# Kernel optimization log

Measured on AMD Instinct MI355X. Metric: run time of the kernel, lower is better.

Reference implementation:

```python
import jax, jax.numpy as jnp
import numpy as np

B, L, E, H = 8, 2048, 1024, 16
D = E // H
EPS = 1e-6


def setup_inputs() -> dict:
    key = jax.random.key(0)
    ks = jax.random.split(key, 9)
    s = 1.0 / np.sqrt(E)
    def lin_w(k):
        return jax.random.uniform(k, (E, E), jnp.float32, -s, s)
    def lin_b(k):
        return jax.random.uniform(k, (E,), jnp.float32, -s, s)
    return {
        "query": jax.random.normal(ks[0], (B, L, E), jnp.float32),
        "Wq": lin_w(ks[1]), "bq": lin_b(ks[2]),
        "Wk": lin_w(ks[3]), "bk": lin_b(ks[4]),
        "Wv": lin_w(ks[5]), "bv": lin_b(ks[6]),
        "Wo": lin_w(ks[7]), "bo": lin_b(ks[8]),
    }


def reference(query, Wq, bq, Wk, bk, Wv, bv, Wo, bo):
    bsz, tgt_len, embed_dim = query.shape
    n_head = H
    head_dim = embed_dim // n_head
    m = tgt_len  # src_len == tgt_len (self-attention)

    # projections (torch Linear with W stored as (in, out) here)
    q = query @ Wq + bq
    k = query @ Wk + bk
    v = query @ Wv + bv

    # (B, L, E) -> (B, H, L, D), softmax feature map over head dim
    def to_heads(x):
        return x.reshape(bsz, tgt_len, n_head, head_dim).transpose(0, 2, 1, 3)

    q = jax.nn.softmax(to_heads(q), axis=-1)
    k = jax.nn.softmax(to_heads(k), axis=-1)
    v = to_heads(v)
    comp_q = 1.0 - q
    comp_k = 1.0 - k

    # cosFormer positional reweighting: idx = (pi/2) * (1..m) / m
    idx = (np.pi / 2) * jnp.arange(1, m + 1, dtype=jnp.float32) / m  # (L,)
    sin = jnp.sin(idx)[None, None, :, None]  # (1,1,L,1)
    cos = jnp.cos(idx)[None, None, :, None]

    def feat(x):  # (B,H,L,D) -> (B,H,L,2D)
        return jnp.concatenate([x * sin, x * cos], axis=-1)

    qf, comp_qf = feat(q), feat(comp_q)
    kf, comp_kf = feat(k), feat(comp_k)

    def branch(qf_, kf_):
        kv = jnp.einsum('bhld,bhlm->bhdm', kf_, v)            # (B,H,2D,D)
        z = 1.0 / jnp.maximum(
            jnp.einsum('bhld,bhd->bhl', qf_, kf_.sum(axis=2)), EPS)
        return jnp.einsum('bhld,bhdm,bhl->bhlm', qf_, kv, z)  # (B,H,L,D)

    attn = branch(qf, kf) + branch(comp_qf, comp_kf)

    # torch: (B*H,L,D).transpose(0,1).view(L,B,E)
    out = attn.transpose(2, 0, 1, 3).reshape(tgt_len, bsz, embed_dim)
    out = out @ Wo + bo
    # torch final: .view(bsz, tgt_len, n_feat) -- raw reshape, no transpose
    return out.reshape(bsz, tgt_len, embed_dim)
```

## Files before the change

kernel.cpp:

```cpp
#include <hip/hip_runtime.h>
#include <hip/hip_bf16.h>
#include <cstdint>

#define B_   8
#define L_   2048
#define E_   1024
#define H_   16
#define D_   64
#define M_   (B_ * L_)
#define EPS_ 1e-6f
#define PI2_ 1.57079632679f

typedef __bf16 bf16;
typedef __bf16 bf16x8 __attribute__((ext_vector_type(8)));
typedef __bf16 bf16x4 __attribute__((ext_vector_type(4)));
typedef float  floatx4 __attribute__((ext_vector_type(4)));

__device__ inline void async_cp16(const void* g, void* l) {
  __builtin_amdgcn_global_load_lds(
      (__attribute__((address_space(1))) void*)const_cast<void*>(g),
      (__attribute__((address_space(3))) void*)l,
      16, 0, 0);
}

__global__ __launch_bounds__(256) void k_convert_x(const float* __restrict__ x,
                                                   bf16* __restrict__ o) {
  size_t i = ((size_t)blockIdx.x * 256 + threadIdx.x) * 8;
  floatx4 a = *(const floatx4*)(x + i);
  floatx4 b = *(const floatx4*)(x + i + 4);
  bf16x8 r;
  r[0] = (bf16)a[0]; r[1] = (bf16)a[1]; r[2] = (bf16)a[2]; r[3] = (bf16)a[3];
  r[4] = (bf16)b[0]; r[5] = (bf16)b[1]; r[6] = (bf16)b[2]; r[7] = (bf16)b[3];
  *(bf16x8*)(o + i) = r;
}

struct TArgs { const float* src[4]; bf16* dst[4]; };

__global__ __launch_bounds__(256) void k_transpose_w(TArgs t) {
  __shared__ float tile[32][33];
  const float* src = t.src[blockIdx.z];
  bf16* dst = t.dst[blockIdx.z];
  int bx = blockIdx.x, by = blockIdx.y;
  int x = threadIdx.x, y = threadIdx.y;
#pragma unroll
  for (int i = 0; i < 4; i++) {
    int r = by * 32 + y + i * 8;
    tile[y + i * 8][x] = src[(size_t)r * E_ + bx * 32 + x];
  }
  __syncthreads();
#pragma unroll
  for (int i = 0; i < 4; i++) {
    int r = bx * 32 + y + i * 8;
    dst[(size_t)r * E_ + by * 32 + x] = (bf16)tile[x][y + i * 8];
  }
}

#define BAR()   asm volatile("s_barrier" ::: "memory")
#define LGKM0() asm volatile("s_waitcnt lgkmcnt(0)" ::: "memory")
#define VMW4()  asm volatile("s_waitcnt vmcnt(4)" ::: "memory")
#define VMW0()  asm volatile("s_waitcnt vmcnt(0)" ::: "memory")
#define MFMA_   __builtin_amdgcn_mfma_f32_16x16x32_bf16

#define GEMM_TILE(t_, c_) {                                                    \
    const int t = (t_); const int c = (c_);                                    \
    bf16x8 a0[4][2], a1[4][2], b0[2][2], b1[2][2];                             \
                                                                  \
    _Pragma("unroll") for (int i = 0; i < 4; i++) {                            \
      a0[i][0] = RDA(c, 0, i); a0[i][1] = RDA(c, 1, i); }                      \
    _Pragma("unroll") for (int j = 0; j < 2; j++) {                            \
      b0[j][0] = RDB(c, 0, j); b0[j][1] = RDB(c, 1, j); }                      \
    if (t + 1 < 16) STAGE(c ^ 1, 0, t + 1, 0);                                 \
    BAR(); LGKM0();                                                            \
    __builtin_amdgcn_s_setprio(1);                                             \
    _Pragma("unroll") for (int i = 0; i < 4; i++)                              \
      _Pragma("unroll") for (int j = 0; j < 2; j++) {                          \
        acc[i][j] = MFMA_(a0[i][0], b0[j][0], acc[i][j], 0, 0, 0);             \
        acc[i][j] = MFMA_(a0[i][1], b0[j][1], acc[i][j], 0, 0, 0); }           \
    __builtin_amdgcn_s_setprio(0);                                             \
    BAR();                                                                     \
                                                                  \
    _Pragma("unroll") for (int j = 0; j < 2; j++) {                            \
      b1[j][0] = RDB(c, 0, j + 2); b1[j][1] = RDB(c, 1, j + 2); }              \
    if (t + 1 < 16) STAGE(c ^ 1, 0, t + 1, 1);                                 \
    BAR(); LGKM0();                                                            \
    __builtin_amdgcn_s_setprio(1);                                             \
    _Pragma("unroll") for (int i = 0; i < 4; i++)                              \
      _Pragma("unroll") for (int j = 0; j < 2; j++) {                          \
        acc[i][j + 2] = MFMA_(a0[i][0], b1[j][0], acc[i][j + 2], 0, 0, 0);     \
        acc[i][j + 2] = MFMA_(a0[i][1], b1[j][1], acc[i][j + 2], 0, 0, 0); }   \
    __builtin_amdgcn_s_setprio(0);                                             \
    BAR();                                                                     \
                                                                  \
    _Pragma("unroll") for (int i = 0; i < 4; i++) {                            \
      a1[i][0] = RDA(c, 0, i + 4); a1[i][1] = RDA(c, 1, i + 4); }              \
    if (t + 2 < 16) STAGE(c, 1, t + 2, 0);                                     \
    BAR(); LGKM0();                                                            \
    __builtin_amdgcn_s_setprio(1);                                             \
    _Pragma("unroll") for (int i = 0; i < 4; i++)                              \
      _Pragma("unroll") for (int j = 0; j < 2; j++) {                          \
        acc[i + 4][j + 2] = MFMA_(a1[i][0], b1[j][0], acc[i + 4][j + 2], 0, 0, 0); \
        acc[i + 4][j + 2] = MFMA_(a1[i][1], b1[j][1], acc[i + 4][j + 2], 0, 0, 0); } \
    __builtin_amdgcn_s_setprio(0);                                             \
    BAR();                                                                     \
                                                                  \
    if (t < 14) { STAGE(c, 1, t + 2, 1); VMW4(); } else { VMW0(); }            \
    BAR();                                                                     \
    __builtin_amdgcn_s_setprio(1);                                             \
    _Pragma("unroll") for (int i = 0; i < 4; i++)                              \
      _Pragma("unroll") for (int j = 0; j < 2; j++) {                          \
        acc[i + 4][j] = MFMA_(a1[i][0], b0[j][0], acc[i + 4][j], 0, 0, 0);     \
        acc[i + 4][j] = MFMA_(a1[i][1], b0[j][1], acc[i + 4][j], 0, 0, 0); }   \
    __builtin_amdgcn_s_setprio(0);                                             \
    BAR();                                                                     \
  }

__device__ __forceinline__ void gemm256_core(const bf16* __restrict__ Agl,
                                             const bf16* __restrict__ Bgl,
                                             int bm, int bn, bf16* ldsb,
                                             floatx4 (&acc)[8][4]) {
  const int tid  = threadIdx.x;
  const int wid  = tid >> 6;
  const int lane = tid & 63;
  const int quad = lane >> 4;
  const int l15  = lane & 15;
  const int wm   = wid >> 2;
  const int wn   = wid & 3;
  const int rb   = wn * 32;
  const int gcol = wm * 32 + (((lane & 3) * 8) ^ ((lane & 32) ? 16 : 0));
  const bf16* pA = Agl + (size_t)(bm * 256 + rb + (lane >> 2)) * E_ + gcol;
  const bf16* pB = Bgl + (size_t)(bn * 256 + rb + (lane >> 2)) * E_ + gcol;
  const int aCol = (quad * 8) ^ ((l15 & 8) ? 16 : 0);

  auto LDSP = [&](int c, int mat, int qq, int row, int col) -> bf16* {
    return ldsb + ((((c * 2 + mat) * 2 + qq) * 256 + row) * 32 + col);
  };
  auto STAGE = [&](int c, int mat, int tt, int h) {
    const bf16* g = (mat ? pB : pA) + (size_t)(h * 128) * E_ + tt * 64;
    bf16* lp = LDSP(c, mat, wm, h * 128 + rb, 0);
    async_cp16(g, lp);
    async_cp16(g + (size_t)16 * E_, lp + 16 * 32);
  };
  auto RDA = [&](int c, int qq, int i) -> bf16x8 {
    return *(const bf16x8*)LDSP(c, 0, qq, wm * 128 + i * 16 + l15, aCol);
  };
  auto RDB = [&](int c, int qq, int j) -> bf16x8 {
    return *(const bf16x8*)LDSP(c, 1, qq, wn * 64 + j * 16 + l15, aCol);
  };

  STAGE(0, 1, 0, 0); STAGE(0, 1, 0, 1);
  STAGE(0, 0, 0, 0); STAGE(0, 0, 0, 1);
  STAGE(1, 1, 1, 0); STAGE(1, 1, 1, 1);
  VMW4();
  BAR();

#pragma unroll 1
  for (int tb = 0; tb < 16; tb += 2) {
    GEMM_TILE(tb, 0)
    GEMM_TILE(tb + 1, 1)
  }
}

__global__ __launch_bounds__(512, 2) void k_gemm_qkv256(
    const bf16* __restrict__ A, const bf16* __restrict__ Wt,
    const float* __restrict__ bq, const float* __restrict__ bk,
    const float* __restrict__ bv,
    float* __restrict__ QT, float* __restrict__ KT, bf16* __restrict__ VT) {
  __shared__ __attribute__((aligned(16))) bf16 ldsb[2 * 2 * 2 * 256 * 32];
  const int id  = blockIdx.x;
  const int xcd = id & 7, rr = id >> 3;
  const int bm  = xcd * 8 + rr / 12;
  const int cz  = rr % 12;
  const int bn  = cz & 3, z = cz >> 2;
  const bf16* Bgl = Wt + (size_t)z * E_ * E_;

  floatx4 acc[8][4] = {};
  gemm256_core(A, Bgl, bm, bn, ldsb, acc);

  const int tid  = threadIdx.x;
  const int wid  = tid >> 6;
  const int lane = tid & 63;
  const int quad = lane >> 4;
  const int l15  = lane & 15;
  const int wm   = wid >> 2, wn = wid & 3;
  const float* bias = (z == 0) ? bq : (z == 1) ? bk : bv;
#pragma unroll
  for (int i = 0; i < 8; i++)
#pragma unroll
    for (int j = 0; j < 4; j++) {
      const int col  = bn * 256 + wn * 64 + j * 16 + l15;
      const int row0 = bm * 256 + wm * 128 + i * 16 + quad * 4;
      const int h = col >> 6, d = col & 63;
      const int b = row0 >> 11, l = row0 & 2047;
      const float bb = bias[col];
      floatx4 v = acc[i][j];
      v[0] += bb; v[1] += bb; v[2] += bb; v[3] += bb;
      if (z == 0) {
        *(floatx4*)&QT[(((size_t)(b * 16 + h) * 64 + d) * 2048) + l] = v;
      } else if (z == 1) {
        *(floatx4*)&KT[(((size_t)(b * 16 + h) * 64 + d) * 2048) + l] = v;
      } else {
        bf16x4 rv;
        rv[0] = (bf16)v[0]; rv[1] = (bf16)v[1];
        rv[2] = (bf16)v[2]; rv[3] = (bf16)v[3];
        *(bf16x4*)&VT[(((size_t)(b * 16 + h) * 64 + d) * 2048) + l] = rv;
      }
    }
}

__global__ __launch_bounds__(512, 2) void k_gemm_final256(
    const bf16* __restrict__ A, const bf16* __restrict__ Bt,
    const float* __restrict__ bias, float* __restrict__ C) {
  __shared__ __attribute__((aligned(16))) bf16 ldsb[2 * 2 * 2 * 256 * 32];
  const int id  = blockIdx.x;
  const int xcd = id & 7, rr = id >> 3;
  const int bm  = xcd * 8 + (rr >> 2);
  const int bn  = rr & 3;

  floatx4 acc[8][4] = {};
  gemm256_core(A, Bt, bm, bn, ldsb, acc);

  const int tid  = threadIdx.x;
  const int wid  = tid >> 6;
  const int lane = tid & 63;
  const int quad = lane >> 4;
  const int l15  = lane & 15;
  const int wm   = wid >> 2, wn = wid & 3;
#pragma unroll
  for (int i = 0; i < 8; i++)
#pragma unroll
    for (int j = 0; j < 4; j++) {
      const int col = bn * 256 + wn * 64 + j * 16 + l15;
      const float bb = bias[col];
#pragma unroll
      for (int r = 0; r < 4; r++) {
        const int row = bm * 256 + wm * 128 + i * 16 + quad * 4 + r;
        C[(size_t)row * E_ + col] = acc[i][j][r] + bb;
      }
    }
}

#define AST 40
__global__ __launch_bounds__(256) void k_kv(const float* __restrict__ KT,
                                            const bf16* __restrict__ VT,
                                            float* __restrict__ kvp) {
  __shared__ __attribute__((aligned(16))) float kt[64 * 32];
  __shared__ __attribute__((aligned(16))) bf16  vt[64 * 32];
  __shared__ __attribute__((aligned(16))) bf16  Abuf[128 * AST];
  const int kseg = blockIdx.x;
  const int bh   = blockIdx.y;
  const int t = threadIdx.x;
  const int wid = t >> 6, lane = t & 63;
  const int quad = lane >> 4, l15 = lane & 15;
  const int wm = wid >> 1, wn = wid & 1;
  const int c = t >> 3, ii = t & 7;

  const float* ktg = KT + (size_t)bh * 64 * 2048;
  const bf16*  vtg = VT + (size_t)bh * 64 * 2048;

  floatx4 acc[4][2] = {};
  float rs = 0.f;

  for (int it = 0; it < 16; it++) {
    const int l0 = kseg * 512 + it * 32;
    {
      const int r = lane >> 3, ch = lane & 7;
      const float* g0 = ktg + (size_t)(wid * 16 + r) * 2048 + l0 + ch * 4;
      const float* g1 = ktg + (size_t)(wid * 16 + 8 + r) * 2048 + l0 + ch * 4;
      async_cp16(g0, &kt[(wid * 16) * 32]);
      async_cp16(g1, &kt[(wid * 16 + 8) * 32]);
    }
    {
      const int r = lane >> 2, ch = lane & 3;
      const bf16* g0 = vtg + (size_t)(wid * 16 + r) * 2048 + l0 + ch * 8;
      async_cp16(g0, &vt[(wid * 16) * 32]);
    }
    __syncthreads();

    float xv[8];
#pragma unroll
    for (int j = 0; j < 8; j++) xv[j] = kt[(ii + 8 * j) * 32 + c];
    float mx = xv[0];
#pragma unroll
    for (int j = 1; j < 8; j++) mx = fmaxf(mx, xv[j]);
    mx = fmaxf(mx, __shfl_xor(mx, 1));
    mx = fmaxf(mx, __shfl_xor(mx, 2));
    mx = fmaxf(mx, __shfl_xor(mx, 4));
    float s = 0.f;
#pragma unroll
    for (int j = 0; j < 8; j++) { xv[j] = __expf(xv[j] - mx); s += xv[j]; }
    s += __shfl_xor(s, 1); s += __shfl_xor(s, 2); s += __shfl_xor(s, 4);
    const float inv = 1.f / s;
    const int l = l0 + c;
    const float ang = PI2_ * (float)(l + 1) / (float)L_;
    const float sn = __sinf(ang), cs = __cosf(ang);
#pragma unroll
    for (int j = 0; j < 8; j++) {
      const float p = xv[j] * inv;
      const int f = ii + 8 * j;
      Abuf[f * AST + c]        = (bf16)(p * sn);
      Abuf[(64 + f) * AST + c] = (bf16)(p * cs);
    }
    __syncthreads();

    if (t < 128) {
      float r8 = 0.f;
#pragma unroll
      for (int g = 0; g < 4; g++) {
        bf16x8 v = *(const bf16x8*)&Abuf[t * AST + g * 8];
#pragma unroll
        for (int e = 0; e < 8; e++) r8 += (float)v[e];
      }
      rs += r8;
    }

    bf16x8 af[4], bfm[2];
#pragma unroll
    for (int i = 0; i < 4; i++)
      af[i] = *(const bf16x8*)&Abuf[(wm * 64 + i * 16 + l15) * AST + quad * 8];
#pragma unroll
    for (int j = 0; j < 2; j++)
      bfm[j] = *(const bf16x8*)&vt[(wn * 32 + j * 16 + l15) * 32 + quad * 8];
#pragma unroll
    for (int i = 0; i < 4; i++)
#pragma unroll
      for (int j = 0; j < 2; j++)
        acc[i][j] = __builtin_amdgcn_mfma_f32_16x16x32_bf16(af[i], bfm[j], acc[i][j], 0, 0, 0);
    __syncthreads();
  }

  float* C = kvp + (size_t)(kseg * 128 + bh) * 128 * 68;
#pragma unroll
  for (int i = 0; i < 4; i++)
#pragma unroll
    for (int j = 0; j < 2; j++) {
      const int col = wn * 32 + j * 16 + l15;
#pragma unroll
      for (int r = 0; r < 4; r++) {
        const int row = wm * 64 + i * 16 + quad * 4 + r;
        C[(size_t)row * 68 + col] = acc[i][j][r];
      }
    }
  if (t < 128) C[(size_t)t * 68 + 64] = rs;
}

__global__ __launch_bounds__(64) void k_consts(const float* __restrict__ kvp,
                                               bf16* __restrict__ KVT,
                                               float* __restrict__ ksbuf) {
  const int bh = blockIdx.x;
  const int dp = threadIdx.x;
  const size_t gs = (size_t)128 * 128 * 68;
  const float* P = kvp + (size_t)bh * 128 * 68;
  bf16* kr = KVT + (size_t)(bh * 64 + dp) * 160;
  float sk0 = 0.f, sk1 = 0.f;
#pragma unroll 8
  for (int f = 0; f < 128; f++) {
    float v = P[(size_t)f * 68 + dp] + P[gs + (size_t)f * 68 + dp]
            + P[2 * gs + (size_t)f * 68 + dp] + P[3 * gs + (size_t)f * 68 + dp];
    kr[f] = (bf16)v;
    if (f < 64) sk0 += v; else sk1 += v;
  }
  float ks0 = P[(size_t)dp * 68 + 64] + P[gs + (size_t)dp * 68 + 64]
            + P[2 * gs + (size_t)dp * 68 + 64] + P[3 * gs + (size_t)dp * 68 + 64];
  float ks1 = P[(size_t)(64 + dp) * 68 + 64] + P[gs + (size_t)(64 + dp) * 68 + 64]
            + P[2 * gs + (size_t)(64 + dp) * 68 + 64] + P[3 * gs + (size_t)(64 + dp) * 68 + 64];
  ksbuf[(size_t)bh * 136 + dp]      = ks0;
  ksbuf[(size_t)bh * 136 + 64 + dp] = ks1;
  float sks0 = ks0, sks1 = ks1;
#pragma unroll
  for (int o = 1; o < 64; o <<= 1) { sks0 += __shfl_xor(sks0, o); sks1 += __shfl_xor(sks1, o); }
  kr[128] = (bf16)(62.f * sk0);
  kr[129] = (bf16)(62.f * sk1);
#pragma unroll
  for (int f = 130; f < 160; f++) kr[f] = (bf16)0.f;
  if (dp == 0) {
    ksbuf[(size_t)bh * 136 + 128] = sks0;
    ksbuf[(size_t)bh * 136 + 129] = sks1;
  }
}

#define ASTR 168
__global__ __launch_bounds__(256) void k_attn(const float* __restrict__ QT,
                                              const bf16* __restrict__ KVT,
                                              const float* __restrict__ ksbuf,
                                              bf16* __restrict__ attn) {
  __shared__ __attribute__((aligned(16))) bf16 Abuf[128 * ASTR];
  __shared__ __attribute__((aligned(16))) bf16 Bbuf[64 * ASTR];
  __shared__ float ksl[136];
  const int lc = blockIdx.x;
  const int bh = blockIdx.y;
  const int b = bh >> 4, h = bh & 15;
  const int t = threadIdx.x;

  {
    const bf16* src = KVT + (size_t)bh * 64 * 160;
#pragma unroll
    for (int i = 0; i < 5; i++) {
      const int idx = t + i * 256;
      const int row = idx / 20, ch = idx % 20;
      *(bf16x8*)&Bbuf[row * ASTR + ch * 8] = *(const bf16x8*)(src + row * 160 + ch * 8);
    }
    if (t < 130) ksl[t] = ksbuf[(size_t)bh * 136 + t];
  }
  __syncthreads();

  if (t < 128) {
    const int l = lc * 128 + t;
    const float* qp = QT + ((size_t)bh * 64) * 2048 + l;
    float xv[64];
#pragma unroll
    for (int d = 0; d < 64; d++) xv[d] = qp[(size_t)d * 2048];
    float mx = -1e30f;
#pragma unroll
    for (int d = 0; d < 64; d++) mx = fmaxf(mx, xv[d]);
    float s = 0.f;
#pragma unroll
    for (int d = 0; d < 64; d++) { xv[d] = __expf(xv[d] - mx); s += xv[d]; }
    const float inv = 1.f / s;
    float t0 = 0.f, t1 = 0.f;
#pragma unroll
    for (int d = 0; d < 64; d++) {
      xv[d] *= inv;
      t0 += xv[d] * ksl[d];
      t1 += xv[d] * ksl[64 + d];
    }
    const float SKS0 = ksl[128], SKS1 = ksl[129];
    const float ang = PI2_ * (float)(l + 1) / (float)L_;
    const float sn = __sinf(ang), cs = __cosf(ang);
    const float den1 = sn * t0 + cs * t1;
    const float den2 = sn * (62.f * SKS0 + t0) + cs * (62.f * SKS1 + t1);
    const float z1 = 1.f / fmaxf(den1, EPS_);
    const float z2 = 1.f / fmaxf(den2, EPS_);
    const float zz = z1 + z2;
    const float a0 = zz * sn, a1 = zz * cs;
    bf16* ar = &Abuf[t * ASTR];
#pragma unroll
    for (int g = 0; g < 8; g++) {
      bf16x8 w;
#pragma unroll
      for (int j = 0; j < 8; j++) w[j] = (bf16)(a0 * xv[g * 8 + j]);
      *(bf16x8*)(ar + g * 8) = w;
    }
#pragma unroll
    for (int g = 0; g < 8; g++) {
      bf16x8 w;
#pragma unroll
      for (int j = 0; j < 8; j++) w[j] = (bf16)(a1 * xv[g * 8 + j]);
      *(bf16x8*)(ar + 64 + g * 8) = w;
    }
    bf16x8 wt = {};
    wt[0] = (bf16)(z2 * sn); wt[1] = (bf16)(z2 * cs);
    *(bf16x8*)(ar + 128) = wt;
    bf16x8 zr = {};
    *(bf16x8*)(ar + 136) = zr;
    *(bf16x8*)(ar + 144) = zr;
    *(bf16x8*)(ar + 152) = zr;
  }
  __syncthreads();

  const int wid = t >> 6, lane = t & 63;
  const int quad = lane >> 4, l15 = lane & 15;
  const int wm = wid >> 1, wn = wid & 1;
  floatx4 acc[4][2] = {};
#pragma unroll
  for (int kk = 0; kk < 5; kk++) {
    bf16x8 af[4], bfm[2];
#pragma unroll
    for (int i = 0; i < 4; i++)
      af[i] = *(const bf16x8*)&Abuf[(wm * 64 + i * 16 + l15) * ASTR + kk * 32 + quad * 8];
#pragma unroll
    for (int j = 0; j < 2; j++)
      bfm[j] = *(const bf16x8*)&Bbuf[(wn * 32 + j * 16 + l15) * ASTR + kk * 32 + quad * 8];
#pragma unroll
    for (int i = 0; i < 4; i++)
#pragma unroll
      for (int j = 0; j < 2; j++)
        acc[i][j] = __builtin_amdgcn_mfma_f32_16x16x32_bf16(af[i], bfm[j], acc[i][j], 0, 0, 0);
  }
#pragma unroll
  for (int i = 0; i < 4; i++)
#pragma unroll
    for (int j = 0; j < 2; j++) {
      const int dp = wn * 32 + j * 16 + l15;
#pragma unroll
      for (int r = 0; r < 4; r++) {
        const int l = lc * 128 + wm * 64 + i * 16 + quad * 4 + r;
        attn[((size_t)l * B_ + b) * E_ + h * 64 + dp] = (bf16)acc[i][j][r];
      }
    }
}

extern "C" void kernel_launch(void* const* d_in, const int* in_sizes, int n_in,
                              void* d_out, int out_size, void* d_ws, size_t ws_size,
                              hipStream_t stream) {
  (void)in_sizes; (void)n_in; (void)out_size; (void)ws_size;
  const float* query = (const float*)d_in[0];
  const float* Wq = (const float*)d_in[1];
  const float* bq = (const float*)d_in[2];
  const float* Wk = (const float*)d_in[3];
  const float* bk = (const float*)d_in[4];
  const float* Wv = (const float*)d_in[5];
  const float* bv = (const float*)d_in[6];
  const float* Wo = (const float*)d_in[7];
  const float* bo = (const float*)d_in[8];

  char* ws = (char*)d_ws;
  float* QT   = (float*)(ws + 0);
  float* KT   = (float*)(ws + 67108864);
  bf16*  VT   = (bf16*) (ws + 134217728);
  bf16*  Wt   = (bf16*) (ws + 167772160);
  bf16*  Xbf  = (bf16*) (ws + 176160768);
  bf16*  attnb= (bf16*) (ws + 176160768);
  float* kvp  = (float*)(ws + 209715200);
  bf16*  KVT  = (bf16*) (ws + 227540992);
  float* ksbuf= (float*)(ws + 230162432);

  k_convert_x<<<(M_ * E_) / (256 * 8), 256, 0, stream>>>(query, Xbf);

  TArgs ta;
  ta.src[0] = Wq; ta.src[1] = Wk; ta.src[2] = Wv; ta.src[3] = Wo;
  ta.dst[0] = Wt;                       ta.dst[1] = Wt + (size_t)E_ * E_;
  ta.dst[2] = Wt + (size_t)2 * E_ * E_; ta.dst[3] = Wt + (size_t)3 * E_ * E_;
  k_transpose_w<<<dim3(32, 32, 4), dim3(32, 8), 0, stream>>>(ta);

  k_gemm_qkv256<<<768, 512, 0, stream>>>(Xbf, Wt, bq, bk, bv, QT, KT, VT);

  k_kv<<<dim3(4, 128), 256, 0, stream>>>(KT, VT, kvp);

  k_consts<<<128, 64, 0, stream>>>(kvp, KVT, ksbuf);

  k_attn<<<dim3(16, 128), 256, 0, stream>>>(QT, KVT, ksbuf, attnb);

  k_gemm_final256<<<256, 512, 0, stream>>>(attnb, Wt + (size_t)3 * E_ * E_, bo, (float*)d_out);
}
```

Before: 362.8 us.

## Fuse Q/K head softmax into QKV GEMM epilogue and store Q/K as bf16

The per-head softmax over the head dimension for Q and K now runs inside the QKV GEMM epilogue, using cross-lane shuffles across the 16-lane groups that hold a 64-wide head. Q and K are written as bf16 instead of fp32, which halves their write and read traffic. The kv kernel is restructured to fold the sin/cos weights into V rather than K and uses swizzled LDS loads. The attention kernel drops its own softmax. The cost is lower precision for the softmaxed Q/K features and a heavier GEMM epilogue.

```diff
diff --git a/kernel.cpp b/kernel.cpp
--- a/kernel.cpp
+++ b/kernel.cpp
@@ -164,7 +164,7 @@
     const bf16* __restrict__ A, const bf16* __restrict__ Wt,
     const float* __restrict__ bq, const float* __restrict__ bk,
     const float* __restrict__ bv,
-    float* __restrict__ QT, float* __restrict__ KT, bf16* __restrict__ VT) {
+    bf16* __restrict__ QTb, bf16* __restrict__ KTb, bf16* __restrict__ VT) {
   __shared__ __attribute__((aligned(16))) bf16 ldsb[2 * 2 * 2 * 256 * 32];
   const int id  = blockIdx.x;
   const int xcd = id & 7, rr = id >> 3;
@@ -183,27 +183,56 @@
   const int l15  = lane & 15;
   const int wm   = wid >> 2, wn = wid & 3;
   const float* bias = (z == 0) ? bq : (z == 1) ? bk : bv;
+  float bb[4];
+#pragma unroll
+  for (int j = 0; j < 4; j++) bb[j] = bias[bn * 256 + wn * 64 + j * 16 + l15];
+
+  if (z < 2) {
+#pragma unroll
+    for (int i = 0; i < 8; i++)
+#pragma unroll
+      for (int r = 0; r < 4; r++) {
+        float v0 = acc[i][0][r] + bb[0];
+        float v1 = acc[i][1][r] + bb[1];
+        float v2 = acc[i][2][r] + bb[2];
+        float v3 = acc[i][3][r] + bb[3];
+        float m = fmaxf(fmaxf(v0, v1), fmaxf(v2, v3));
+        m = fmaxf(m, __shfl_xor(m, 1));
+        m = fmaxf(m, __shfl_xor(m, 2));
+        m = fmaxf(m, __shfl_xor(m, 4));
+        m = fmaxf(m, __shfl_xor(m, 8));
+        v0 = __expf(v0 - m); v1 = __expf(v1 - m);
+        v2 = __expf(v2 - m); v3 = __expf(v3 - m);
+        float s = v0 + v1 + v2 + v3;
+        s += __shfl_xor(s, 1); s += __shfl_xor(s, 2);
+        s += __shfl_xor(s, 4); s += __shfl_xor(s, 8);
+        const float inv = 1.f / s;
+        acc[i][0][r] = v0 * inv; acc[i][1][r] = v1 * inv;
+        acc[i][2][r] = v2 * inv; acc[i][3][r] = v3 * inv;
+      }
+  } else {
+#pragma unroll
+    for (int i = 0; i < 8; i++)
+#pragma unroll
+      for (int j = 0; j < 4; j++) {
+        acc[i][j][0] += bb[j]; acc[i][j][1] += bb[j];
+        acc[i][j][2] += bb[j]; acc[i][j][3] += bb[j];
+      }
+  }
+
+  bf16* OT = (z == 0) ? QTb : (z == 1) ? KTb : VT;
 #pragma unroll
   for (int i = 0; i < 8; i++)
 #pragma unroll
     for (int j = 0; j < 4; j++) {
-      const int col  = bn * 256 + wn * 64 + j * 16 + l15;
-      const int row0 = bm * 256 + wm * 128 + i * 16 + quad * 4;
-      const int h = col >> 6, d = col & 63;
-      const int b = row0 >> 11, l = row0 & 2047;
-      const float bb = bias[col];
-      floatx4 v = acc[i][j];
-      v[0] += bb; v[1] += bb; v[2] += bb; v[3] += bb;
-      if (z == 0) {
-        *(floatx4*)&QT[(((size_t)(b * 16 + h) * 64 + d) * 2048) + l] = v;
-      } else if (z == 1) {
-        *(floatx4*)&KT[(((size_t)(b * 16 + h) * 64 + d) * 2048) + l] = v;
-      } else {
-        bf16x4 rv;
-        rv[0] = (bf16)v[0]; rv[1] = (bf16)v[1];
-        rv[2] = (bf16)v[2]; rv[3] = (bf16)v[3];
-        *(bf16x4*)&VT[(((size_t)(b * 16 + h) * 64 + d) * 2048) + l] = rv;
-      }
+      const int c  = bn * 256 + wn * 64 + j * 16 + l15;
+      const int r0 = bm * 256 + wm * 128 + i * 16 + quad * 4;
+      const int h = c >> 6, d = c & 63;
+      const int b = r0 >> 11, l = r0 & 2047;
+      bf16x4 rv;
+      rv[0] = (bf16)acc[i][j][0]; rv[1] = (bf16)acc[i][j][1];
+      rv[2] = (bf16)acc[i][j][2]; rv[3] = (bf16)acc[i][j][3];
+      *(bf16x4*)&OT[(((size_t)(b * 16 + h) * 64 + d) * 2048) + l] = rv;
     }
 }
 
@@ -239,87 +268,78 @@
     }
 }
 
-#define AST 40
-__global__ __launch_bounds__(256) void k_kv(const float* __restrict__ KT,
+__global__ __launch_bounds__(256) void k_kv(const bf16* __restrict__ KTb,
                                             const bf16* __restrict__ VT,
                                             float* __restrict__ kvp) {
-  __shared__ __attribute__((aligned(16))) float kt[64 * 32];
-  __shared__ __attribute__((aligned(16))) bf16  vt[64 * 32];
-  __shared__ __attribute__((aligned(16))) bf16  Abuf[128 * AST];
+  __shared__ __attribute__((aligned(16))) bf16 ktb[64 * 32];
+  __shared__ __attribute__((aligned(16))) bf16 vt[64 * 32];
+  __shared__ __attribute__((aligned(16))) bf16 Bsn[64 * 40];
+  __shared__ __attribute__((aligned(16))) bf16 Bcs[64 * 40];
+  __shared__ float snl[32], csl[32];
   const int kseg = blockIdx.x;
   const int bh   = blockIdx.y;
   const int t = threadIdx.x;
   const int wid = t >> 6, lane = t & 63;
   const int quad = lane >> 4, l15 = lane & 15;
   const int wm = wid >> 1, wn = wid & 1;
-  const int c = t >> 3, ii = t & 7;
-
-  const float* ktg = KT + (size_t)bh * 64 * 2048;
-  const bf16*  vtg = VT + (size_t)bh * 64 * 2048;
+
+  const bf16* ktg = KTb + (size_t)bh * 64 * 2048;
+  const bf16* vtg = VT  + (size_t)bh * 64 * 2048;
 
   floatx4 acc[4][2] = {};
   float rs = 0.f;
+  const int d_ = t & 63, h_ = t >> 6;
 
   for (int it = 0; it < 16; it++) {
     const int l0 = kseg * 512 + it * 32;
     {
-      const int r = lane >> 3, ch = lane & 7;
-      const float* g0 = ktg + (size_t)(wid * 16 + r) * 2048 + l0 + ch * 4;
-      const float* g1 = ktg + (size_t)(wid * 16 + 8 + r) * 2048 + l0 + ch * 4;
-      async_cp16(g0, &kt[(wid * 16) * 32]);
-      async_cp16(g1, &kt[(wid * 16 + 8) * 32]);
-    }
+      const int r = lane >> 2, ch = lane & 3;
+      const bf16* gk = ktg + (size_t)(wid * 16 + r) * 2048 + l0 + ((ch ^ (r & 1)) * 8);
+      async_cp16(gk, &ktb[(wid * 16) * 32]);
+      const bf16* gv = vtg + (size_t)(wid * 16 + r) * 2048 + l0 + ch * 8;
+      async_cp16(gv, &vt[(wid * 16) * 32]);
+    }
+    if (t < 32) {
+      const float ang = PI2_ * (float)(l0 + t + 1) / (float)L_;
+      snl[t] = __sinf(ang); csl[t] = __cosf(ang);
+    }
+    __syncthreads();
+
     {
-      const int r = lane >> 2, ch = lane & 3;
-      const bf16* g0 = vtg + (size_t)(wid * 16 + r) * 2048 + l0 + ch * 8;
-      async_cp16(g0, &vt[(wid * 16) * 32]);
-    }
-    __syncthreads();
-
-    float xv[8];
-#pragma unroll
-    for (int j = 0; j < 8; j++) xv[j] = kt[(ii + 8 * j) * 32 + c];
-    float mx = xv[0];
-#pragma unroll
-    for (int j = 1; j < 8; j++) mx = fmaxf(mx, xv[j]);
-    mx = fmaxf(mx, __shfl_xor(mx, 1));
-    mx = fmaxf(mx, __shfl_xor(mx, 2));
-    mx = fmaxf(mx, __shfl_xor(mx, 4));
-    float s = 0.f;
-#pragma unroll
-    for (int j = 0; j < 8; j++) { xv[j] = __expf(xv[j] - mx); s += xv[j]; }
-    s += __shfl_xor(s, 1); s += __shfl_xor(s, 2); s += __shfl_xor(s, 4);
-    const float inv = 1.f / s;
-    const int l = l0 + c;
-    const float ang = PI2_ * (float)(l + 1) / (float)L_;
-    const float sn = __sinf(ang), cs = __cosf(ang);
-#pragma unroll
-    for (int j = 0; j < 8; j++) {
-      const float p = xv[j] * inv;
-      const int f = ii + 8 * j;
-      Abuf[f * AST + c]        = (bf16)(p * sn);
-      Abuf[(64 + f) * AST + c] = (bf16)(p * cs);
-    }
-    __syncthreads();
-
+      const int row = t >> 2, cc = (t & 3) * 8;
+      bf16x8 v = *(const bf16x8*)&vt[row * 32 + cc];
+      bf16x8 a, b;
+#pragma unroll
+      for (int e = 0; e < 8; e++) {
+        const float f = (float)v[e];
+        a[e] = (bf16)(f * snl[cc + e]);
+        b[e] = (bf16)(f * csl[cc + e]);
+      }
+      *(bf16x8*)&Bsn[row * 40 + cc] = a;
+      *(bf16x8*)&Bcs[row * 40 + cc] = b;
+    }
     if (t < 128) {
       float r8 = 0.f;
 #pragma unroll
-      for (int g = 0; g < 4; g++) {
-        bf16x8 v = *(const bf16x8*)&Abuf[t * AST + g * 8];
-#pragma unroll
-        for (int e = 0; e < 8; e++) r8 += (float)v[e];
+      for (int p = 0; p < 4; p++) {
+        bf16x8 v = *(const bf16x8*)&ktb[d_ * 32 + p * 8];
+        const int gl = (p ^ (d_ & 1)) * 8;
+#pragma unroll
+        for (int e = 0; e < 8; e++)
+          r8 += (float)v[e] * (h_ ? csl[gl + e] : snl[gl + e]);
       }
       rs += r8;
     }
+    __syncthreads();
 
     bf16x8 af[4], bfm[2];
+    const bf16* Bsel = wm ? Bcs : Bsn;
 #pragma unroll
     for (int i = 0; i < 4; i++)
-      af[i] = *(const bf16x8*)&Abuf[(wm * 64 + i * 16 + l15) * AST + quad * 8];
+      af[i] = *(const bf16x8*)&ktb[(i * 16 + l15) * 32 + ((quad ^ (l15 & 1)) * 8)];
 #pragma unroll
     for (int j = 0; j < 2; j++)
-      bfm[j] = *(const bf16x8*)&vt[(wn * 32 + j * 16 + l15) * 32 + quad * 8];
+      bfm[j] = *(const bf16x8*)&Bsel[(wn * 32 + j * 16 + l15) * 40 + quad * 8];
 #pragma unroll
     for (int i = 0; i < 4; i++)
 #pragma unroll
@@ -379,7 +399,7 @@
 }
 
 #define ASTR 168
-__global__ __launch_bounds__(256) void k_attn(const float* __restrict__ QT,
+__global__ __launch_bounds__(256) void k_attn(const bf16* __restrict__ QTb,
                                               const bf16* __restrict__ KVT,
                                               const float* __restrict__ ksbuf,
                                               bf16* __restrict__ attn) {
@@ -405,21 +425,13 @@
 
   if (t < 128) {
     const int l = lc * 128 + t;
-    const float* qp = QT + ((size_t)bh * 64) * 2048 + l;
+    const bf16* qp = QTb + (size_t)bh * 64 * 2048 + l;
     float xv[64];
 #pragma unroll
-    for (int d = 0; d < 64; d++) xv[d] = qp[(size_t)d * 2048];
-    float mx = -1e30f;
-#pragma unroll
-    for (int d = 0; d < 64; d++) mx = fmaxf(mx, xv[d]);
-    float s = 0.f;
-#pragma unroll
-    for (int d = 0; d < 64; d++) { xv[d] = __expf(xv[d] - mx); s += xv[d]; }
-    const float inv = 1.f / s;
+    for (int d = 0; d < 64; d++) xv[d] = (float)qp[(size_t)d * 2048];
     float t0 = 0.f, t1 = 0.f;
 #pragma unroll
     for (int d = 0; d < 64; d++) {
-      xv[d] *= inv;
       t0 += xv[d] * ksl[d];
       t1 += xv[d] * ksl[64 + d];
     }
@@ -504,15 +516,15 @@
   const float* bo = (const float*)d_in[8];
 
   char* ws = (char*)d_ws;
-  float* QT   = (float*)(ws + 0);
-  float* KT   = (float*)(ws + 67108864);
-  bf16*  VT   = (bf16*) (ws + 134217728);
-  bf16*  Wt   = (bf16*) (ws + 167772160);
-  bf16*  Xbf  = (bf16*) (ws + 176160768);
-  bf16*  attnb= (bf16*) (ws + 176160768);
-  float* kvp  = (float*)(ws + 209715200);
-  bf16*  KVT  = (bf16*) (ws + 227540992);
-  float* ksbuf= (float*)(ws + 230162432);
+  bf16*  QTb  = (bf16*) (ws + 0);
+  bf16*  KTb  = (bf16*) (ws + 33554432);
+  bf16*  VT   = (bf16*) (ws + 67108864);
+  bf16*  Wt   = (bf16*) (ws + 100663296);
+  bf16*  Xbf  = (bf16*) (ws + 109051904);
+  bf16*  attnb= (bf16*) (ws + 109051904);
+  float* kvp  = (float*)(ws + 142606336);
+  bf16*  KVT  = (bf16*) (ws + 160432128);
+  float* ksbuf= (float*)(ws + 163053568);
 
   k_convert_x<<<(M_ * E_) / (256 * 8), 256, 0, stream>>>(query, Xbf);
 
@@ -522,13 +534,13 @@
   ta.dst[2] = Wt + (size_t)2 * E_ * E_; ta.dst[3] = Wt + (size_t)3 * E_ * E_;
   k_transpose_w<<<dim3(32, 32, 4), dim3(32, 8), 0, stream>>>(ta);
 
-  k_gemm_qkv256<<<768, 512, 0, stream>>>(Xbf, Wt, bq, bk, bv, QT, KT, VT);
-
-  k_kv<<<dim3(4, 128), 256, 0, stream>>>(KT, VT, kvp);
+  k_gemm_qkv256<<<768, 512, 0, stream>>>(Xbf, Wt, bq, bk, bv, QTb, KTb, VT);
+
+  k_kv<<<dim3(4, 128), 256, 0, stream>>>(KTb, VT, kvp);
 
   k_consts<<<128, 64, 0, stream>>>(kvp, KVT, ksbuf);
 
-  k_attn<<<dim3(16, 128), 256, 0, stream>>>(QT, KVT, ksbuf, attnb);
+  k_attn<<<dim3(16, 128), 256, 0, stream>>>(QTb, KVT, ksbuf, attnb);
 
   k_gemm_final256<<<256, 512, 0, stream>>>(attnb, Wt + (size_t)3 * E_ * E_, bo, (float*)d_out);
 }
```

New measurement: 374.3 us. +3.2%, slower.
